# Performance work log

Hardware: AMD Instinct MI355X
Metric: run time of the kernel (lower is better)

The kernel has to match this reference:

```python
import jax, jax.numpy as jnp
import numpy as np

# Model dims (match init_kwargs / input_specs)
L, D, H, F = 4, 1024, 16, 4096   # layers, d_model, heads, ffn hidden
B, S = 4, 1024                    # batch, seq_len
HD = D // H                       # head dim = 64
K = 8                             # context-mask band width (k=8, 2//k == 0)
LN_EPS = 1e-5


def setup_inputs():
    key = jax.random.key(0)
    ks = jax.random.split(key, 16)
    s = 0.02  # init scale for weights
    return {
        "src":   jax.random.normal(ks[0], (B, S, D), jnp.float32),
        # stacked per-layer params (leading dim L)
        "Wqkv":  jax.random.normal(ks[1], (L, 3 * D, D), jnp.float32) * s,
        "bqkv":  jnp.zeros((L, 3 * D), jnp.float32),
        "Wo":    jax.random.normal(ks[2], (L, D, D), jnp.float32) * s,
        "bo":    jnp.zeros((L, D), jnp.float32),
        "W1":    jax.random.normal(ks[3], (L, F, D), jnp.float32) * s,
        "b1":    jnp.zeros((L, F), jnp.float32),
        "W2":    jax.random.normal(ks[4], (L, D, F), jnp.float32) * s,
        "b2":    jnp.zeros((L, D), jnp.float32),
        "ln1_w": jnp.ones((L, D), jnp.float32),
        "ln1_b": jnp.zeros((L, D), jnp.float32),
        "ln2_w": jnp.ones((L, D), jnp.float32),
        "ln2_b": jnp.zeros((L, D), jnp.float32),
    }


def _layer_norm(x, g, b):
    m = jnp.mean(x, axis=-1, keepdims=True)
    v = jnp.mean(jnp.square(x - m), axis=-1, keepdims=True)
    return (x - m) * jax.lax.rsqrt(v + LN_EPS) * g + b


def _context_mask(sz):
    # row i allows keys j with i <= j < i + K (clamped into range); 0 allowed, -inf masked
    i = jnp.arange(sz)[:, None]
    j = jnp.arange(sz)[None, :]
    return jnp.where((j >= i) & (j < i + K), 0.0, -jnp.inf).astype(jnp.float32)


def reference(src, Wqkv, bqkv, Wo, bo, W1, b1, W2, b2, ln1_w, ln1_b, ln2_w, ln2_b):
    mask = _context_mask(S)  # [S, S] additive mask
    scale = 1.0 / jnp.sqrt(jnp.float32(HD))
    x = src  # [B, S, D] (batch-first; equivalent to torch's permute round-trip)
    for l in range(L):
        # --- self-attention (post-norm, dropout=0) ---
        qkv = jnp.einsum('bsd,ed->bse', x, Wqkv[l]) + bqkv[l]  # [B,S,3D]
        q, k, v = jnp.split(qkv, 3, axis=-1)
        q = q.reshape(B, S, H, HD).transpose(0, 2, 1, 3)  # [B,H,S,HD]
        k = k.reshape(B, S, H, HD).transpose(0, 2, 1, 3)
        v = v.reshape(B, S, H, HD).transpose(0, 2, 1, 3)
        scores = jnp.einsum('bhqd,bhkd->bhqk', q, k) * scale + mask
        attn = jax.nn.softmax(scores, axis=-1)
        o = jnp.einsum('bhqk,bhkd->bhqd', attn, v)
        o = o.transpose(0, 2, 1, 3).reshape(B, S, D)
        o = jnp.einsum('bsd,ed->bse', o, Wo[l]) + bo[l]
        x = _layer_norm(x + o, ln1_w[l], ln1_b[l])
        # --- feed-forward, exact (erf) gelu ---
        h = jax.nn.gelu(jnp.einsum('bsd,fd->bsf', x, W1[l]) + b1[l], approximate=False)
        h = jnp.einsum('bsf,df->bsd', h, W2[l]) + b2[l]
        x = _layer_norm(x + h, ln2_w[l], ln2_b[l])
    return x
```

## Files before the change

### kernel.cpp

```cpp
#include <hip/hip_runtime.h>

#define LNUM 4
#define DMODEL 1024
#define NHEAD 16
#define FDIM 4096
#define BATCH 4
#define SEQ 1024
#define HDIM 64
#define KBAND 8
#define MROWS (BATCH * SEQ)

typedef __attribute__((ext_vector_type(8))) __bf16 bf16x8;
typedef __attribute__((ext_vector_type(4))) float f32x4;
typedef __attribute__((ext_vector_type(8))) unsigned short u16x8;

__device__ __forceinline__ unsigned short f2bf(float f) {
  unsigned int u = __builtin_bit_cast(unsigned int, f);
  u = u + 0x7fffu + ((u >> 16) & 1u);
  return (unsigned short)(u >> 16);
}
__device__ __forceinline__ float bf2f(unsigned short h) {
  unsigned int u = ((unsigned int)h) << 16;
  return __builtin_bit_cast(float, u);
}

#define GLOAD16(gp, lp)                                                        \
  __builtin_amdgcn_global_load_lds(                                            \
      (const __attribute__((address_space(1))) void*)(gp),                     \
      (__attribute__((address_space(3))) void*)(lp), 16, 0, 0)

__global__ __launch_bounds__(256) void cvt_bf16(const float* __restrict__ in,
                                                unsigned short* __restrict__ out,
                                                long n) {
  long i = ((long)blockIdx.x * 256 + threadIdx.x) * 4;
  if (i + 3 < n) {
    float4 v = *reinterpret_cast<const float4*>(in + i);
    ushort4 o;
    o.x = f2bf(v.x);
    o.y = f2bf(v.y);
    o.z = f2bf(v.z);
    o.w = f2bf(v.w);
    *reinterpret_cast<ushort4*>(out + i) = o;
  }
}

template <int EPI>
__global__ __launch_bounds__(256, 3) void gemm128(const unsigned short* __restrict__ A,
                                                  const unsigned short* __restrict__ W,
                                                  const float* __restrict__ bias,
                                                  unsigned short* __restrict__ Cout,
                                                  int Ndim, int Kdim, int Ks) {
  __shared__ unsigned short SH[16384];
  const int tid = threadIdx.x;
  const int wave = tid >> 6;
  const int lane = tid & 63;

  const int gx = gridDim.x, gy = gridDim.y;
  const int nwg = gx * gy;
  const int lin = blockIdx.x + blockIdx.y * gx;
  const int q8 = nwg >> 3, r8 = nwg & 7;
  const int xcd = lin & 7, cidx = lin >> 3;
  const int cbase = (xcd < r8) ? xcd * (q8 + 1) : r8 * (q8 + 1) + (xcd - r8) * q8;
  const int swz = cbase + cidx;
  const int bm0 = (swz % gy) * 128;
  const int bn0 = (swz / gy) * 128;
  const int kz0 = blockIdx.z * Ks;

  const int r0 = tid >> 2;
  const int c0 = (((tid & 3) ^ ((tid >> 3) & 3)) << 3);
  const unsigned short* gA = A + (size_t)(bm0 + r0) * Kdim + kz0 + c0;
  const unsigned short* gB = W + (size_t)(bn0 + r0) * Kdim + kz0 + c0;
  const size_t rowstep = (size_t)64 * Kdim;

  f32x4 acc[4][4] = {};

  const int wr = (wave >> 1) * 64;
  const int wc = (wave & 1) * 64;
  const int fr = lane & 15;
  const int kg = lane >> 4;
  const int kofs = ((kg ^ ((fr >> 1) & 3)) << 3);

#define STAGE(buf, kt)                                                         \
  do {                                                                         \
    const unsigned short* pa = gA + (size_t)(kt) * 32;                         \
    const unsigned short* pb = gB + (size_t)(kt) * 32;                         \
    unsigned short* la = &SH[(buf) * 8192];                                    \
    unsigned short* lb = &SH[(buf) * 8192 + 4096];                             \
    GLOAD16(pa, la + wave * 512);                                              \
    GLOAD16(pa + rowstep, la + 2048 + wave * 512);                             \
    GLOAD16(pb, lb + wave * 512);                                              \
    GLOAD16(pb + rowstep, lb + 2048 + wave * 512);                             \
  } while (0)

  const int nt = Ks >> 5;
  STAGE(0, 0);
  for (int t = 0; t < nt; ++t) {
    const int cur = t & 1;
    if (t + 1 < nt) {
      STAGE(cur ^ 1, t + 1);
      asm volatile("s_waitcnt vmcnt(4)" ::: "memory");
    } else {
      asm volatile("s_waitcnt vmcnt(0)" ::: "memory");
    }
    __builtin_amdgcn_s_barrier();
    asm volatile("" ::: "memory");
    const unsigned short* As = &SH[cur * 8192];
    const unsigned short* Bs = &SH[cur * 8192 + 4096];
    bf16x8 af[4], bfr[4];
#pragma unroll
    for (int i = 0; i < 4; ++i)
      af[i] = *reinterpret_cast<const bf16x8*>(&As[(wr + i * 16 + fr) * 32 + kofs]);
#pragma unroll
    for (int j = 0; j < 4; ++j)
      bfr[j] = *reinterpret_cast<const bf16x8*>(&Bs[(wc + j * 16 + fr) * 32 + kofs]);
#pragma unroll
    for (int i = 0; i < 4; ++i)
#pragma unroll
      for (int j = 0; j < 4; ++j)
        acc[i][j] = __builtin_amdgcn_mfma_f32_16x16x32_bf16(af[i], bfr[j], acc[i][j], 0, 0, 0);
    asm volatile("" ::: "memory");
    __builtin_amdgcn_s_barrier();
  }
#undef STAGE

  const int rr = (lane >> 4) * 4;
  const int cc = lane & 15;
  const bool addb = (EPI != 2) || (blockIdx.z == 0);
  unsigned short* outZ =
      Cout + (EPI == 2 ? (size_t)blockIdx.z * ((size_t)gy * 128) * Ndim : 0);
  float bv[4];
#pragma unroll
  for (int j = 0; j < 4; ++j)
    bv[j] = addb ? bias[bn0 + wc + j * 16 + cc] : 0.0f;

  unsigned short* lt = SH + wave * 1280;
#pragma unroll
  for (int rh = 0; rh < 2; ++rh) {
#pragma unroll
    for (int cp = 0; cp < 2; ++cp) {
#pragma unroll
      for (int ii = 0; ii < 2; ++ii)
#pragma unroll
        for (int jj = 0; jj < 2; ++jj)
#pragma unroll
          for (int r = 0; r < 4; ++r) {
            float v = acc[rh * 2 + ii][cp * 2 + jj][r] + bv[cp * 2 + jj];
            if (EPI == 1) v = 0.5f * v * (1.0f + erff(v * 0.70710678118654752f));
            lt[(ii * 16 + rr + r) * 40 + jj * 16 + cc] = f2bf(v);
          }
      asm volatile("s_waitcnt lgkmcnt(0)" ::: "memory");
      const int rl = lane >> 1;
      const int chalf = (lane & 1) * 16;
      u16x8 o0 = *reinterpret_cast<const u16x8*>(&lt[rl * 40 + chalf]);
      u16x8 o1 = *reinterpret_cast<const u16x8*>(&lt[rl * 40 + chalf + 8]);
      const int m = bm0 + wr + rh * 32 + rl;
      const int n0 = bn0 + wc + cp * 32 + chalf;
      unsigned short* dst = outZ + (size_t)m * Ndim + n0;
      *reinterpret_cast<u16x8*>(dst) = o0;
      *reinterpret_cast<u16x8*>(dst + 8) = o1;
      asm volatile("s_waitcnt lgkmcnt(0)" ::: "memory");
    }
  }
}

__global__ __launch_bounds__(256) void attn_band(const unsigned short* __restrict__ qkv,
                                                 unsigned short* __restrict__ outp) {
  const int gw = blockIdx.x * 4 + (threadIdx.x >> 6);
  const int lane = threadIdx.x & 63;
  const int q = gw & (SEQ - 1);
  const int bh = gw >> 10;
  const int h = bh & (NHEAD - 1);
  const int b = bh >> 4;
  const size_t row0 = (size_t)(b * SEQ + q);
  const size_t stride = 3 * DMODEL;
  const float qv = bf2f(qkv[row0 * stride + h * HDIM + lane]);

  float sc[KBAND];
  float mx = -1e30f;
#pragma unroll
  for (int jj = 0; jj < KBAND; ++jj) {
    const int j = q + jj;
    const int jc = (j < SEQ) ? j : (SEQ - 1);
    float kv = bf2f(qkv[(size_t)(b * SEQ + jc) * stride + DMODEL + h * HDIM + lane]);
    float p = qv * kv;
#pragma unroll
    for (int m = 32; m; m >>= 1) p += __shfl_xor(p, m);
    p *= 0.125f;
    p = (j < SEQ) ? p : -1e30f;
    sc[jj] = p;
    mx = fmaxf(mx, p);
  }
  float denom = 0.f;
  float ov = 0.f;
#pragma unroll
  for (int jj = 0; jj < KBAND; ++jj) {
    const int j = q + jj;
    const int jc = (j < SEQ) ? j : (SEQ - 1);
    float p = __expf(sc[jj] - mx);
    p = (j < SEQ) ? p : 0.f;
    denom += p;
    ov += p * bf2f(qkv[(size_t)(b * SEQ + jc) * stride + 2 * DMODEL + h * HDIM + lane]);
  }
  ov /= denom;
  outp[row0 * DMODEL + h * HDIM + lane] = f2bf(ov);
}

__global__ __launch_bounds__(256) void add_ln(const float* __restrict__ resid,
                                              const unsigned short* __restrict__ part,
                                              int nz,
                                              const float* __restrict__ gw,
                                              const float* __restrict__ gb,
                                              float* __restrict__ xf,
                                              unsigned short* __restrict__ xb) {
  const int row = blockIdx.x;
  const int tid = threadIdx.x;
  const size_t slab = (size_t)MROWS * DMODEL;
  const float* rp = resid + (size_t)row * DMODEL;
  const unsigned short* pp = part + (size_t)row * DMODEL;
  float v[4];
  float s = 0.f, s2 = 0.f;
#pragma unroll
  for (int i = 0; i < 4; ++i) {
    const int idx = tid + i * 256;
    float a = rp[idx];
    for (int z = 0; z < nz; ++z) a += bf2f(pp[z * slab + idx]);
    v[i] = a;
    s += a;
    s2 += a * a;
  }
#pragma unroll
  for (int m = 32; m; m >>= 1) {
    s += __shfl_xor(s, m);
    s2 += __shfl_xor(s2, m);
  }
  __shared__ float wsm[8];
  const int wave = tid >> 6, lane = tid & 63;
  if (lane == 0) {
    wsm[wave] = s;
    wsm[4 + wave] = s2;
  }
  __syncthreads();
  s = wsm[0] + wsm[1] + wsm[2] + wsm[3];
  s2 = wsm[4] + wsm[5] + wsm[6] + wsm[7];
  const float mean = s * (1.f / DMODEL);
  const float var = s2 * (1.f / DMODEL) - mean * mean;
  const float rstd = rsqrtf(var + 1e-5f);
#pragma unroll
  for (int i = 0; i < 4; ++i) {
    const int idx = tid + i * 256;
    const float y = (v[i] - mean) * rstd * gw[idx] + gb[idx];
    xf[(size_t)row * DMODEL + idx] = y;
    xb[(size_t)row * DMODEL + idx] = f2bf(y);
  }
}

extern "C" void kernel_launch(void* const* d_in, const int* in_sizes, int n_in,
                              void* d_out, int out_size, void* d_ws, size_t ws_size,
                              hipStream_t stream) {
  const float* src  = (const float*)d_in[0];
  const float* Wqkv = (const float*)d_in[1];
  const float* bqkv = (const float*)d_in[2];
  const float* Wo   = (const float*)d_in[3];
  const float* bo   = (const float*)d_in[4];
  const float* W1   = (const float*)d_in[5];
  const float* b1   = (const float*)d_in[6];
  const float* W2   = (const float*)d_in[7];
  const float* b2   = (const float*)d_in[8];
  const float* ln1w = (const float*)d_in[9];
  const float* ln1b = (const float*)d_in[10];
  const float* ln2w = (const float*)d_in[11];
  const float* ln2b = (const float*)d_in[12];
  float* out = (float*)d_out;

  char* p = (char*)d_ws;
  unsigned short* wqkv_b = (unsigned short*)p; p += (size_t)LNUM * 3072 * 1024 * 2;
  unsigned short* wo_b   = (unsigned short*)p; p += (size_t)LNUM * 1024 * 1024 * 2;
  unsigned short* w1_b   = (unsigned short*)p; p += (size_t)LNUM * 4096 * 1024 * 2;
  unsigned short* w2_b   = (unsigned short*)p; p += (size_t)LNUM * 1024 * 4096 * 2;
  float*          xf     = (float*)p;          p += (size_t)MROWS * DMODEL * 4;
  unsigned short* xb     = (unsigned short*)p; p += (size_t)MROWS * DMODEL * 2;
  char* R = p;
  unsigned short* qkvb = (unsigned short*)R;
  unsigned short* aob  = (unsigned short*)(R + (size_t)MROWS * 3 * DMODEL * 2);
  unsigned short* hb   = (unsigned short*)R;
  unsigned short* part = (unsigned short*)(R + (size_t)MROWS * 4096 * 2);
  p = R + (size_t)MROWS * 4096 * 2 + (size_t)4 * MROWS * DMODEL * 2;
  if (ws_size < (size_t)(p - (char*)d_ws)) return;

  cvt_bf16<<<(long)LNUM * 3072 * 1024 / 1024, 256, 0, stream>>>(Wqkv, wqkv_b, (long)LNUM * 3072 * 1024);
  cvt_bf16<<<(long)LNUM * 1024 * 1024 / 1024, 256, 0, stream>>>(Wo, wo_b, (long)LNUM * 1024 * 1024);
  cvt_bf16<<<(long)LNUM * 4096 * 1024 / 1024, 256, 0, stream>>>(W1, w1_b, (long)LNUM * 4096 * 1024);
  cvt_bf16<<<(long)LNUM * 1024 * 4096 / 1024, 256, 0, stream>>>(W2, w2_b, (long)LNUM * 1024 * 4096);
  cvt_bf16<<<(long)MROWS * DMODEL / 1024, 256, 0, stream>>>(src, xb, (long)MROWS * DMODEL);

  for (int l = 0; l < LNUM; ++l) {
    gemm128<0><<<dim3(3072 / 128, MROWS / 128, 1), 256, 0, stream>>>(
        xb, wqkv_b + (size_t)l * 3072 * 1024, bqkv + l * 3072, qkvb, 3072, 1024, 1024);
    attn_band<<<(BATCH * NHEAD * SEQ) / 4, 256, 0, stream>>>(qkvb, aob);
    gemm128<2><<<dim3(1024 / 128, MROWS / 128, 2), 256, 0, stream>>>(
        aob, wo_b + (size_t)l * 1024 * 1024, bo + l * 1024, part, 1024, 1024, 512);
    add_ln<<<MROWS, 256, 0, stream>>>(l == 0 ? src : xf, part, 2,
                                      ln1w + l * DMODEL, ln1b + l * DMODEL, xf, xb);
    gemm128<1><<<dim3(FDIM / 128, MROWS / 128, 1), 256, 0, stream>>>(
        xb, w1_b + (size_t)l * 4096 * 1024, b1 + l * FDIM, hb, FDIM, 1024, 1024);
    gemm128<2><<<dim3(1024 / 128, MROWS / 128, 4), 256, 0, stream>>>(
        hb, w2_b + (size_t)l * 1024 * 4096, b2 + l * 1024, part, 1024, 4096, 1024);
    float* dst = (l == LNUM - 1) ? out : xf;
    add_ln<<<MROWS, 256, 0, stream>>>(xf, part, 4,
                                      ln2w + l * DMODEL, ln2b + l * DMODEL, dst, xb);
  }
}
```

Before: 1.009 ms.

## Drop fp32 residual buffer, super-tile GEMM block mapping, raise occupancy hint

The residual stream is now kept only in bf16. LayerNorm reads and writes the bf16 buffer in place and writes fp32 only for the final output, which removes fp32 residual reads and writes per LayerNorm. GEMM workgroups are remapped into 8x8 super-tiles for better L2 reuse, and the launch-bounds occupancy hint rises from 3 to 4 blocks per CU. This trades residual precision, with bf16 rounding accumulating across layers, and may cause register spills from the tighter register budget.

After: 927.0 us. -8.1%, faster.

```diff
diff --git a/kernel.cpp b/kernel.cpp
--- a/kernel.cpp
+++ b/kernel.cpp
@@ -45,7 +45,7 @@
 }
 
 template <int EPI>
-__global__ __launch_bounds__(256, 3) void gemm128(const unsigned short* __restrict__ A,
+__global__ __launch_bounds__(256, 4) void gemm128(const unsigned short* __restrict__ A,
                                                   const unsigned short* __restrict__ W,
                                                   const float* __restrict__ bias,
                                                   unsigned short* __restrict__ Cout,
@@ -62,8 +62,11 @@
   const int xcd = lin & 7, cidx = lin >> 3;
   const int cbase = (xcd < r8) ? xcd * (q8 + 1) : r8 * (q8 + 1) + (xcd - r8) * q8;
   const int swz = cbase + cidx;
-  const int bm0 = (swz % gy) * 128;
-  const int bn0 = (swz / gy) * 128;
+  const int sup = swz >> 6, inn = swz & 63;
+  const int sbm = sup % (gy >> 3);
+  const int sbn = sup / (gy >> 3);
+  const int bm0 = (sbm * 8 + (inn & 7)) * 128;
+  const int bn0 = (sbn * 8 + (inn >> 3)) * 128;
   const int kz0 = blockIdx.z * Ks;
 
   const int r0 = tid >> 2;
@@ -205,24 +208,24 @@
   outp[row0 * DMODEL + h * HDIM + lane] = f2bf(ov);
 }
 
-__global__ __launch_bounds__(256) void add_ln(const float* __restrict__ resid,
+__global__ __launch_bounds__(256) void add_ln(const float* __restrict__ srcf,
+                                              unsigned short* __restrict__ xb,
                                               const unsigned short* __restrict__ part,
                                               int nz,
                                               const float* __restrict__ gw,
                                               const float* __restrict__ gb,
-                                              float* __restrict__ xf,
-                                              unsigned short* __restrict__ xb) {
+                                              float* __restrict__ outf) {
   const int row = blockIdx.x;
   const int tid = threadIdx.x;
   const size_t slab = (size_t)MROWS * DMODEL;
-  const float* rp = resid + (size_t)row * DMODEL;
+  unsigned short* xp = xb + (size_t)row * DMODEL;
   const unsigned short* pp = part + (size_t)row * DMODEL;
   float v[4];
   float s = 0.f, s2 = 0.f;
 #pragma unroll
   for (int i = 0; i < 4; ++i) {
     const int idx = tid + i * 256;
-    float a = rp[idx];
+    float a = srcf ? srcf[(size_t)row * DMODEL + idx] : bf2f(xp[idx]);
     for (int z = 0; z < nz; ++z) a += bf2f(pp[z * slab + idx]);
     v[i] = a;
     s += a;
@@ -249,8 +252,8 @@
   for (int i = 0; i < 4; ++i) {
     const int idx = tid + i * 256;
     const float y = (v[i] - mean) * rstd * gw[idx] + gb[idx];
-    xf[(size_t)row * DMODEL + idx] = y;
-    xb[(size_t)row * DMODEL + idx] = f2bf(y);
+    xp[idx] = f2bf(y);
+    if (outf) outf[(size_t)row * DMODEL + idx] = y;
   }
 }
 
@@ -277,7 +280,6 @@
   unsigned short* wo_b   = (unsigned short*)p; p += (size_t)LNUM * 1024 * 1024 * 2;
   unsigned short* w1_b   = (unsigned short*)p; p += (size_t)LNUM * 4096 * 1024 * 2;
   unsigned short* w2_b   = (unsigned short*)p; p += (size_t)LNUM * 1024 * 4096 * 2;
-  float*          xf     = (float*)p;          p += (size_t)MROWS * DMODEL * 4;
   unsigned short* xb     = (unsigned short*)p; p += (size_t)MROWS * DMODEL * 2;
   char* R = p;
   unsigned short* qkvb = (unsigned short*)R;
@@ -299,14 +301,14 @@
     attn_band<<<(BATCH * NHEAD * SEQ) / 4, 256, 0, stream>>>(qkvb, aob);
     gemm128<2><<<dim3(1024 / 128, MROWS / 128, 2), 256, 0, stream>>>(
         aob, wo_b + (size_t)l * 1024 * 1024, bo + l * 1024, part, 1024, 1024, 512);
-    add_ln<<<MROWS, 256, 0, stream>>>(l == 0 ? src : xf, part, 2,
-                                      ln1w + l * DMODEL, ln1b + l * DMODEL, xf, xb);
+    add_ln<<<MROWS, 256, 0, stream>>>(l == 0 ? src : nullptr, xb, part, 2,
+                                      ln1w + l * DMODEL, ln1b + l * DMODEL, nullptr);
     gemm128<1><<<dim3(FDIM / 128, MROWS / 128, 1), 256, 0, stream>>>(
         xb, w1_b + (size_t)l * 4096 * 1024, b1 + l * FDIM, hb, FDIM, 1024, 1024);
     gemm128<2><<<dim3(1024 / 128, MROWS / 128, 4), 256, 0, stream>>>(
         hb, w2_b + (size_t)l * 1024 * 4096, b2 + l * 1024, part, 1024, 4096, 1024);
-    float* dst = (l == LNUM - 1) ? out : xf;
-    add_ln<<<MROWS, 256, 0, stream>>>(xf, part, 4,
-                                      ln2w + l * DMODEL, ln2b + l * DMODEL, dst, xb);
-  }
-}
+    add_ln<<<MROWS, 256, 0, stream>>>(nullptr, xb, part, 4,
+                                      ln2w + l * DMODEL, ln2b + l * DMODEL,
+                                      (l == LNUM - 1) ? out : nullptr);
+  }
+}
```
